# Kernel optimization log

Measured on AMD Instinct MI355X. Metric: run time of the kernel, lower is better.

The kernel has to match this reference:

```python
import jax, jax.numpy as jnp
import numpy as np

N = 100000
E = 800000
IN_CH = 128
HID = 32
HEADS = 8
OUT_CH = 40
NEG_SLOPE = 0.2


def setup_inputs() -> dict:
    key = jax.random.key(0)
    ks = jax.random.split(key, 10)
    x = jax.random.normal(ks[0], (N, IN_CH), dtype=jnp.float32)
    edge_index = jax.random.randint(ks[1], (2, E), 0, N, dtype=jnp.int64)
    # GATConv layer 1: in -> heads*hid, concat=True
    s1 = 1.0 / np.sqrt(IN_CH)
    W1 = jax.random.uniform(ks[2], (IN_CH, HEADS * HID), jnp.float32, -s1, s1)
    att_src1 = jax.random.uniform(ks[3], (1, HEADS, HID), jnp.float32, -s1, s1)
    att_dst1 = jax.random.uniform(ks[4], (1, HEADS, HID), jnp.float32, -s1, s1)
    b1 = jnp.zeros((HEADS * HID,), jnp.float32)
    # GATConv layer 2: heads*hid -> out, heads=1, concat=True
    s2 = 1.0 / np.sqrt(HEADS * HID)
    W2 = jax.random.uniform(ks[5], (HEADS * HID, OUT_CH), jnp.float32, -s2, s2)
    att_src2 = jax.random.uniform(ks[6], (1, 1, OUT_CH), jnp.float32, -s2, s2)
    att_dst2 = jax.random.uniform(ks[7], (1, 1, OUT_CH), jnp.float32, -s2, s2)
    b2 = jnp.zeros((OUT_CH,), jnp.float32)
    return {"x": x, "edge_index": edge_index,
            "W1": W1, "att_src1": att_src1, "att_dst1": att_dst1, "b1": b1,
            "W2": W2, "att_src2": att_src2, "att_dst2": att_dst2, "b2": b2}


def _gat_layer(x, src, dst, W, att_src, att_dst, bias, heads, out_ch):
    n = x.shape[0]
    xp = (x @ W).reshape(n, heads, out_ch)               # [N,H,C]
    a_src = jnp.sum(xp * att_src, axis=-1)               # [N,H]
    a_dst = jnp.sum(xp * att_dst, axis=-1)               # [N,H]
    logits = a_src[src] + a_dst[dst]                      # [Etot,H]
    logits = jnp.where(logits > 0, logits, NEG_SLOPE * logits)  # leaky_relu
    # segment softmax over destination node
    m = jax.ops.segment_max(logits, dst, num_segments=n)  # [N,H]
    p = jnp.exp(logits - m[dst])
    z = jax.ops.segment_sum(p, dst, num_segments=n)
    alpha = p / (z[dst] + 1e-16)                           # [Etot,H]
    out = jax.ops.segment_sum(xp[src] * alpha[:, :, None], dst, num_segments=n)
    return out.reshape(n, heads * out_ch) + bias


def reference(x, edge_index, W1, att_src1, att_dst1, b1, W2, att_src2, att_dst2, b2):
    n = x.shape[0]
    # add self loops (PyG GATConv default add_self_loops=True)
    loop = jnp.arange(n, dtype=edge_index.dtype)
    src = jnp.concatenate([edge_index[0], loop])
    dst = jnp.concatenate([edge_index[1], loop])
    # dropout p=0.2 is identity in eval mode
    h = _gat_layer(x, src, dst, W1, att_src1, att_dst1, b1, HEADS, HID)
    h = jax.nn.relu(h)
    out = _gat_layer(h, src, dst, W2, att_src2, att_dst2, b2, 1, OUT_CH)
    return jax.nn.log_softmax(out, axis=1)
```

## Files before the change

kernel.cpp:

```cpp
#include <hip/hip_runtime.h>
#include <math.h>

#define NN 100000
#define NE 800000
#define C1 256
#define OC 40
#define XPAD 64
#define NEG 0.2f
#define FCHUNK 4096
#define G1BLK 782

typedef _Float16 h4 __attribute__((ext_vector_type(4)));
typedef _Float16 h8 __attribute__((ext_vector_type(8)));
typedef float f4v __attribute__((ext_vector_type(4)));
typedef float f2v __attribute__((ext_vector_type(2)));

static __device__ __forceinline__ float leaky(float v){ return v > 0.f ? v : NEG*v; }

static __device__ __forceinline__ h8 mk8(float4 a, float4 b){
  h8 r = {(_Float16)a.x,(_Float16)a.y,(_Float16)a.z,(_Float16)a.w,
          (_Float16)b.x,(_Float16)b.y,(_Float16)b.z,(_Float16)b.w};
  return r;
}

static __device__ __forceinline__ void gload_lds16h(const _Float16* g, _Float16* l){
  __builtin_amdgcn_global_load_lds((const __attribute__((address_space(1))) void*)g,
                                   (__attribute__((address_space(3))) void*)l, 16, 0, 0);
}


__global__ __launch_bounds__(256) void k_wt(const float* __restrict__ W1, const float* __restrict__ W2,
                                            const float* __restrict__ aS1, const float* __restrict__ aD1,
                                            const float* __restrict__ aS2, const float* __restrict__ aD2,
                                            _Float16* __restrict__ W1s, _Float16* __restrict__ W2t,
                                            int* __restrict__ deg){
  int b = blockIdx.x;
  if (b < 128){
    int k = b, c = threadIdx.x;
    W1s[(size_t)c*128 + (((k>>3) ^ (c&15))<<3) + (k&7)] = (_Float16)W1[k*256 + c];
  } else if (b < 176){
    int nb = b - 128;
    int e = threadIdx.x;
    int l = e >> 2, j = e & 3;
    int k = (l>>5)*128 + ((l>>4)&1)*64 + j*16 + (l&15);
    float v = (nb < OC) ? W2[(size_t)k*OC + nb] : 0.f;
    W2t[(size_t)nb*256 + e] = (_Float16)v;
  } else if (b < 178){
    int b2 = b - 176;
    int h  = threadIdx.x >> 5;
    int kb = (threadIdx.x & 31) * 4;
    const float* att = b2 ? aD1 : aS1;
    const int c = 256 + b2*8 + h;
    #pragma unroll
    for (int kk = 0; kk < 4; ++kk){
      int k = kb + kk;
      float s = 0.f;
      for (int cc = 0; cc < 32; ++cc) s += W1[k*256 + h*32 + cc] * att[h*32 + cc];
      W1s[(size_t)c*128 + (((k>>3) ^ (c&15))<<3) + (k&7)] = (_Float16)s;
    }
  } else if (b < 194){
    int j = b - 178;
    int e = threadIdx.x;
    int l = e >> 2, jj = e & 3;
    int k = (l>>5)*128 + ((l>>4)&1)*64 + jj*16 + (l&15);
    float v = 0.f;
    if (j == 0){ for (int c = 0; c < OC; ++c) v += W2[(size_t)k*OC + c] * aS2[c]; }
    else if (j == 1){ for (int c = 0; c < OC; ++c) v += W2[(size_t)k*OC + c] * aD2[c]; }
    W2t[(size_t)(48 + j)*256 + e] = (_Float16)v;
  } else {
    int i = (b - 194)*256 + threadIdx.x;
    if (i < NN) deg[i] = 1;
  }
}

__global__ __launch_bounds__(512, 4) void k_gemm1(const float* __restrict__ x,
    const _Float16* __restrict__ W1s, unsigned* __restrict__ xp1w,
    float* __restrict__ asrc, float* __restrict__ adst,
    const int* __restrict__ ei, int* __restrict__ deg)
{
  __shared__ _Float16 bs[272*128];
  if (blockIdx.x >= G1BLK){
    int i = (blockIdx.x - G1BLK)*512 + threadIdx.x;
    if (i < NE) atomicAdd(&deg[ei[NE + i]], 1);
    return;
  }
  const int tid  = threadIdx.x;
  const int lane = tid & 63;
  const int w    = tid >> 6;
  const int n = lane & 15, quad = lane >> 4;
  const int r0 = blockIdx.x * 128 + w*16;

  #pragma unroll
  for (int it = 0; it < 8; ++it){
    int idx = it*512 + tid;
    gload_lds16h(W1s + (size_t)idx*8, bs + (size_t)(it*512 + w*64)*8);
  }
  if (w < 4){
    int idx = 4096 + w*64 + lane;
    gload_lds16h(W1s + (size_t)idx*8, bs + (size_t)(4096 + w*64)*8);
  }

  int ra = r0 + n; ra = ra < NN ? ra : NN-1;
  const float* xr = x + (size_t)ra*128 + quad*8;
  float4 fa[4][2];
  #pragma unroll
  for (int ks = 0; ks < 4; ++ks){
    fa[ks][0] = *(const float4*)(xr + ks*32);
    fa[ks][1] = *(const float4*)(xr + ks*32 + 4);
  }

  __syncthreads();

  f4v acc[17];
  #pragma unroll
  for (int ct = 0; ct < 17; ++ct) acc[ct] = (f4v){0.f,0.f,0.f,0.f};

  #pragma unroll
  for (int ks = 0; ks < 4; ++ks){
    h8 a = mk8(fa[ks][0], fa[ks][1]);
    #pragma unroll
    for (int ct = 0; ct < 17; ++ct){
      const int col = ct*16 + n;
      h8 b = *((const h8*)bs + (size_t)col*16 + (((ks*4 + quad) ^ n)));
      acc[ct] = __builtin_amdgcn_mfma_f32_16x16x32_f16(a, b, acc[ct], 0, 0, 0);
    }
  }

  #pragma unroll
  for (int reg = 0; reg < 4; ++reg){
    const int row = r0 + quad*4 + reg;
    if (row < NN){
      float v[16];
      #pragma unroll
      for (int ct = 0; ct < 16; ++ct) v[ct] = acc[ct][reg];
      unsigned dw0 = (unsigned)__builtin_amdgcn_cvt_pk_fp8_f32(v[0], v[1], 0, false);
      dw0 = (unsigned)__builtin_amdgcn_cvt_pk_fp8_f32(v[2], v[3], (int)dw0, true);
      unsigned dw1 = (unsigned)__builtin_amdgcn_cvt_pk_fp8_f32(v[4], v[5], 0, false);
      dw1 = (unsigned)__builtin_amdgcn_cvt_pk_fp8_f32(v[6], v[7], (int)dw1, true);
      unsigned dw2 = (unsigned)__builtin_amdgcn_cvt_pk_fp8_f32(v[8], v[9], 0, false);
      dw2 = (unsigned)__builtin_amdgcn_cvt_pk_fp8_f32(v[10], v[11], (int)dw2, true);
      unsigned dw3 = (unsigned)__builtin_amdgcn_cvt_pk_fp8_f32(v[12], v[13], 0, false);
      dw3 = (unsigned)__builtin_amdgcn_cvt_pk_fp8_f32(v[14], v[15], (int)dw3, true);
      unsigned* xw = xp1w + (size_t)row*64;
      xw[n]      = dw0;
      xw[16 + n] = dw1;
      xw[32 + n] = dw2;
      xw[48 + n] = dw3;
      float vE = acc[16][reg];
      if (n < 8) asrc[row*8 + n] = vE;
      else       adst[row*8 + (n - 8)] = vE;
    }
  }
}

__global__ __launch_bounds__(256) void k_scan1(const int* __restrict__ deg, int* part, int* bsum){
  __shared__ int lds[256];
  const int t = threadIdx.x;
  const int base = blockIdx.x*1024;
  int v[4]; int s = 0;
  #pragma unroll
  for (int i = 0; i < 4; ++i){ int idx = base + t*4 + i; v[i] = (idx < NN) ? deg[idx] : 0; s += v[i]; }
  lds[t] = s; __syncthreads();
  for (int off = 1; off < 256; off <<= 1){
    int xx = (t >= off) ? lds[t-off] : 0;
    __syncthreads();
    lds[t] += xx;
    __syncthreads();
  }
  int excl = lds[t] - s;
  #pragma unroll
  for (int i = 0; i < 4; ++i){ int idx = base + t*4 + i; if (idx < NN) part[idx] = excl; excl += v[i]; }
  if (t == 255) bsum[blockIdx.x] = lds[255];
}
__global__ void k_scan2(const int* __restrict__ bsum, int* boff){
  const int l = threadIdx.x;
  int a = (l      < 98) ? bsum[l]      : 0;
  int b = (64 + l < 98) ? bsum[64 + l] : 0;
  int sa = a, sb = b;
  #pragma unroll
  for (int off = 1; off < 64; off <<= 1){
    int ta = __shfl_up(sa, off, 64);
    int tb = __shfl_up(sb, off, 64);
    if (l >= off){ sa += ta; sb += tb; }
  }
  const int totalA = __shfl(sa, 63, 64);
  if (l      < 98) boff[l]      = sa - a;
  if (64 + l < 98) boff[64 + l] = totalA + sb - b;
}
__global__ __launch_bounds__(256) void k_scan3(const int* __restrict__ part, const int* __restrict__ boff,
                                               int* rowptr, int* cursor){
  int i = blockIdx.x*256 + threadIdx.x;
  if (i < NN){ int v = part[i] + boff[i >> 10]; rowptr[i] = v; cursor[i] = v; }
  if (i == 0) rowptr[NN] = NN + NE;
}
__global__ __launch_bounds__(256) void k_fill(const int* __restrict__ ei, int* cursor, int* __restrict__ esrc){
  const int xcd = blockIdx.x & 7;
  const int base = (blockIdx.x >> 3) * FCHUNK;
  const int lo = xcd * (NN/8), hi = lo + (NN/8);
  const int end = (base + FCHUNK < NE + NN) ? (base + FCHUNK) : (NE + NN);
  for (int i = base + threadIdx.x; i < end; i += 256){
    int s, d;
    if (i < NE){ s = ei[i]; d = ei[NE + i]; } else { s = d = i - NE; }
    if (d >= lo && d < hi){
      int slot = atomicAdd(&cursor[d], 1);
      esrc[slot] = s;
    }
  }
}

template<int B>
static __device__ __forceinline__ void agg1_batch(
    const int j0, const int je, const int lane,
    const int* __restrict__ esrc, const float* __restrict__ asrc,
    const float adA, const float adB,
    const unsigned* __restrict__ xp1w,
    f2v& accLo, f2v& accHi, float& z0, float& z1)
{
  const int cnt = je - j0;
  const int slot = lane & 15;
  const int hA = (lane >> 4) << 1;
  int idx = j0 + slot; idx = idx < je ? idx : je - 1;
  const int sv = esrc[idx];
  float pv0 = 0.f, pv1 = 0.f;
  if (slot < cnt){
    f2v av = *(const f2v*)(asrc + (size_t)sv*8 + hA);
    pv0 = __expf(leaky(av.x + adA));
    pv1 = __expf(leaky(av.y + adB));
  }
  z0 += pv0; z1 += pv1;
  unsigned u[B];
  #pragma unroll
  for (int e = 0; e < B; ++e){
    int s = __builtin_amdgcn_readlane(sv, e);
    u[e] = xp1w[(size_t)s*64 + lane];
  }
  __builtin_amdgcn_sched_barrier(0);
  const int pb = lane & 48;
  #pragma unroll
  for (int e = 0; e < B; ++e){
    const float pA = __shfl(pv0, pb | e, 64);
    const float pB = __shfl(pv1, pb | e, 64);
    f2v lo = __builtin_amdgcn_cvt_pk_f32_fp8((int)u[e], false);
    f2v hi = __builtin_amdgcn_cvt_pk_f32_fp8((int)u[e], true);
    accLo += (f2v){pA, pA} * lo;
    accHi += (f2v){pB, pB} * hi;
  }
}

__global__ __launch_bounds__(1024) void k_agg1(const unsigned* __restrict__ xp1w,
    const float* __restrict__ asrc, const float* __restrict__ adst,
    const float* __restrict__ b1, const int* __restrict__ rowptr,
    const int* __restrict__ esrc, const _Float16* __restrict__ W2t,
    _Float16* __restrict__ xp2, float* __restrict__ asrc2, float* __restrict__ adst2)
{
  __shared__ _Float16 hs[16*264];
  const int lane = threadIdx.x & 63;
  const int w = threadIdx.x >> 6;
  int n = __builtin_amdgcn_readfirstlane(blockIdx.x*16 + w);
  const int hA = (lane >> 4) << 1;
  const f2v ad = *(const f2v*)(adst + (size_t)n*8 + hA);
  const int jb = rowptr[n], je = rowptr[n+1];
  const int cbase = (lane>>5)*128 + ((lane>>4)&1)*64 + (lane&15);
  const float bp0 = b1[cbase], bp1 = b1[cbase+16], bp2 = b1[cbase+32], bp3 = b1[cbase+48];
  f2v accLo = {0.f,0.f}, accHi = {0.f,0.f};
  float z0 = 0.f, z1 = 0.f;

  int j0 = jb;
  while (j0 < je){
    if (je - j0 > 8){
      agg1_batch<16>(j0, je, lane, esrc, asrc, ad.x, ad.y, xp1w, accLo, accHi, z0, z1);
      j0 += 16;
    } else {
      agg1_batch<8>(j0, je, lane, esrc, asrc, ad.x, ad.y, xp1w, accLo, accHi, z0, z1);
      j0 += 8;
    }
  }
  #pragma unroll
  for (int off = 1; off <= 8; off <<= 1){
    z0 += __shfl_xor(z0, off, 64);
    z1 += __shfl_xor(z1, off, 64);
  }
  const float invA = 1.f/(z0 + 1e-16f), invB = 1.f/(z1 + 1e-16f);
  h4 o = {(_Float16)fmaxf(accLo.x*invA + bp0, 0.f),
          (_Float16)fmaxf(accLo.y*invA + bp1, 0.f),
          (_Float16)fmaxf(accHi.x*invB + bp2, 0.f),
          (_Float16)fmaxf(accHi.y*invB + bp3, 0.f)};
  ((h4*)(hs + (size_t)w*264))[lane] = o;

  __syncthreads();

  if (w < 4){
    const int nq = lane & 15, quad = lane >> 4;
    f4v acc = (f4v){0.f,0.f,0.f,0.f};
    #pragma unroll
    for (int ks = 0; ks < 8; ++ks){
      h8 a = *(const h8*)(hs + (size_t)nq*264 + ks*32 + quad*8);
      h8 b = *(const h8*)(W2t + (size_t)(w*16 + nq)*256 + ks*32 + quad*8);
      acc = __builtin_amdgcn_mfma_f32_16x16x32_f16(a, b, acc, 0, 0, 0);
    }
    const int nb = __builtin_amdgcn_readfirstlane(blockIdx.x*16);
    #pragma unroll
    for (int reg = 0; reg < 4; ++reg){
      const int row = nb + quad*4 + reg;
      float v = acc[reg];
      _Float16* xr = xp2 + (size_t)row*XPAD;
      if (w == 0)      xr[nq]      = (_Float16)v;
      else if (w == 1) xr[16 + nq] = (_Float16)v;
      else if (w == 2){ if (nq < 8) xr[32 + nq] = (_Float16)v; }
      else { if (nq == 0) asrc2[row] = v; else if (nq == 1) adst2[row] = v; }
    }
  }
}

__global__ __launch_bounds__(256) void k_agg2(const _Float16* __restrict__ xp2,
    const float* __restrict__ asrc2, const float* __restrict__ adst2,
    const float* __restrict__ b2, const int* __restrict__ rowptr,
    const int* __restrict__ esrc, float* __restrict__ out)
{
  const int lane = threadIdx.x & 63;
  const int g = lane >> 4;
  const int t = lane & 15;
  int n = __builtin_amdgcn_readfirstlane(blockIdx.x*4 + (threadIdx.x >> 6));
  const float ad = adst2[n];
  const int jb = rowptr[n], je = rowptr[n+1];
  f4v acc = {0.f,0.f,0.f,0.f};
  float zacc = 0.f;

  for (int j0 = jb; j0 < je; j0 += 16){
    const int cnt = je - j0;
    int idx = j0 + t; idx = idx < je ? idx : je - 1;
    const int sv = esrc[idx];
    const float pv = (t < cnt) ? __expf(leaky(asrc2[sv] + ad)) : 0.f;
    zacc += pv;
    h4 u[4];
    #pragma unroll
    for (int e4 = 0; e4 < 4; ++e4){
      int svg = __shfl(sv, e4*4 + g, 64);
      u[e4] = *(const h4*)(xp2 + (size_t)svg*XPAD + t*4);
    }
    __builtin_amdgcn_sched_barrier(0);
    #pragma unroll
    for (int e4 = 0; e4 < 4; ++e4){
      const float p = __shfl(pv, e4*4 + g, 64);
      acc.x += p*(float)u[e4].x;
      acc.y += p*(float)u[e4].y;
      acc.z += p*(float)u[e4].z;
      acc.w += p*(float)u[e4].w;
    }
  }
  #pragma unroll
  for (int off = 1; off <= 8; off <<= 1) zacc += __shfl_xor(zacc, off, 64);
  #pragma unroll
  for (int off = 16; off <= 32; off <<= 1){
    acc.x += __shfl_xor(acc.x, off, 64);
    acc.y += __shfl_xor(acc.y, off, 64);
    acc.z += __shfl_xor(acc.z, off, 64);
    acc.w += __shfl_xor(acc.w, off, 64);
  }
  const float inv = 1.f/(zacc + 1e-16f);
  const bool act = t < 10;
  float4 bv = act ? *(const float4*)(b2 + 4*t) : make_float4(0.f,0.f,0.f,0.f);
  float v0 = acc.x*inv + bv.x, v1 = acc.y*inv + bv.y;
  float v2 = acc.z*inv + bv.z, v3 = acc.w*inv + bv.w;
  float m = act ? fmaxf(fmaxf(v0,v1), fmaxf(v2,v3)) : -INFINITY;
  #pragma unroll
  for (int off = 1; off <= 8; off <<= 1) m = fmaxf(m, __shfl_xor(m, off, 64));
  float es = act ? (__expf(v0-m)+__expf(v1-m)+__expf(v2-m)+__expf(v3-m)) : 0.f;
  #pragma unroll
  for (int off = 1; off <= 8; off <<= 1) es += __shfl_xor(es, off, 64);
  if (lane < 10){
    float lse = m + __logf(es);
    float4 o = make_float4(v0-lse, v1-lse, v2-lse, v3-lse);
    *(float4*)(out + (size_t)n*OC + 4*t) = o;
  }
}

extern "C" void kernel_launch(void* const* d_in, const int* in_sizes, int n_in,
                              void* d_out, int out_size, void* d_ws, size_t ws_size,
                              hipStream_t stream)
{
  const float* x   = (const float*)d_in[0];
  const int*   ei  = (const int*)  d_in[1];
  const float* W1  = (const float*)d_in[2];
  const float* aS1 = (const float*)d_in[3];
  const float* aD1 = (const float*)d_in[4];
  const float* b1  = (const float*)d_in[5];
  const float* W2  = (const float*)d_in[6];
  const float* aS2 = (const float*)d_in[7];
  const float* aD2 = (const float*)d_in[8];
  const float* b2  = (const float*)d_in[9];
  float* out = (float*)d_out;

  char* wsp = (char*)d_ws;
  size_t off = 0;
  auto alloc = [&](size_t bytes){ void* p = wsp + off; off += (bytes + 255) & ~(size_t)255; return p; };
  unsigned* xp1w = (unsigned*)alloc((size_t)NN*C1);
  float* as1  = (float*)alloc((size_t)NN*8*4);
  float* ad1  = (float*)alloc((size_t)NN*8*4);
  float* as2  = (float*)alloc((size_t)NN*4);
  float* ad2  = (float*)alloc((size_t)NN*4);
  int* deg    = (int*)alloc((size_t)NN*4);
  int* part   = (int*)alloc((size_t)NN*4);
  int* rowptr = (int*)alloc((size_t)(NN+1)*4);
  int* cursor = (int*)alloc((size_t)NN*4);
  int* bsum   = (int*)alloc(98*4);
  int* boff   = (int*)alloc(98*4);
  int* esrc   = (int*)alloc((size_t)(NN+NE)*4);
  _Float16* W1s = (_Float16*)alloc((size_t)272*128*2);
  _Float16* W2t = (_Float16*)alloc((size_t)64*256*2);
  _Float16* xp2 = (_Float16*)alloc((size_t)NN*XPAD*2);
  (void)ws_size; (void)in_sizes; (void)n_in; (void)out_size;

  const int fill_chunks = (NE + NN + FCHUNK - 1) / FCHUNK;
  const int deg_blocks  = (NE + 511) / 512;

  k_wt    <<<194 + (NN + 255)/256, 256, 0, stream>>>(W1, W2, aS1, aD1, aS2, aD2, W1s, W2t, deg);
  k_gemm1 <<<G1BLK + deg_blocks,   512, 0, stream>>>(x, W1s, xp1w, as1, ad1, ei, deg);
  k_scan1 <<<98,   256, 0, stream>>>(deg, part, bsum);
  k_scan2 <<<1,    64,  0, stream>>>(bsum, boff);
  k_scan3 <<<391,  256, 0, stream>>>(part, boff, rowptr, cursor);
  k_fill  <<<fill_chunks*8, 256, 0, stream>>>(ei, cursor, esrc);
  k_agg1  <<<6250, 1024, 0, stream>>>(xp1w, as1, ad1, b1, rowptr, esrc, W2t, xp2, as2, ad2);
  k_agg2  <<<25000,256, 0, stream>>>(xp2, as2, ad2, b2, rowptr, esrc, out);
}
```

Measured before the change: 308.5 us.

## Sort nodes by in-degree bucket to balance aggregation warps

Builds a degree histogram during the scan, prefix-sums it, and produces a permutation of nodes grouped by in-degree (capped at 63). Both aggregation kernels then process nodes in that permuted order, so the waves in a block handle similar edge counts and spend less time idling on divergent loop lengths. This adds histogram atomics, a perm array and an extra indirection. Nodes sharing a block are no longer adjacent, so layer-2 output writes become scattered and reads of destination-side data lose locality.

```diff
diff --git a/kernel.cpp b/kernel.cpp
--- a/kernel.cpp
+++ b/kernel.cpp
@@ -33,7 +33,7 @@
                                             const float* __restrict__ aS1, const float* __restrict__ aD1,
                                             const float* __restrict__ aS2, const float* __restrict__ aD2,
                                             _Float16* __restrict__ W1s, _Float16* __restrict__ W2t,
-                                            int* __restrict__ deg){
+                                            int* __restrict__ deg, int* __restrict__ hbin){
   int b = blockIdx.x;
   if (b < 128){
     int k = b, c = threadIdx.x;
@@ -70,6 +70,7 @@
   } else {
     int i = (b - 194)*256 + threadIdx.x;
     if (i < NN) deg[i] = 1;
+    if (b == 194 && threadIdx.x < 64) hbin[threadIdx.x] = 0;
   }
 }
 
@@ -153,14 +154,22 @@
   }
 }
 
-__global__ __launch_bounds__(256) void k_scan1(const int* __restrict__ deg, int* part, int* bsum){
+__global__ __launch_bounds__(256) void k_scan1(const int* __restrict__ deg, int* part, int* bsum,
+                                               int* __restrict__ hbin){
   __shared__ int lds[256];
+  __shared__ int lh[64];
   const int t = threadIdx.x;
+  if (t < 64) lh[t] = 0;
   const int base = blockIdx.x*1024;
   int v[4]; int s = 0;
   #pragma unroll
   for (int i = 0; i < 4; ++i){ int idx = base + t*4 + i; v[i] = (idx < NN) ? deg[idx] : 0; s += v[i]; }
   lds[t] = s; __syncthreads();
+  #pragma unroll
+  for (int i = 0; i < 4; ++i){
+    int idx = base + t*4 + i;
+    if (idx < NN) atomicAdd(&lh[v[i] < 63 ? v[i] : 63], 1);
+  }
   for (int off = 1; off < 256; off <<= 1){
     int xx = (t >= off) ? lds[t-off] : 0;
     __syncthreads();
@@ -171,8 +180,11 @@
   #pragma unroll
   for (int i = 0; i < 4; ++i){ int idx = base + t*4 + i; if (idx < NN) part[idx] = excl; excl += v[i]; }
   if (t == 255) bsum[blockIdx.x] = lds[255];
-}
-__global__ void k_scan2(const int* __restrict__ bsum, int* boff){
+  __syncthreads();
+  if (t < 64 && lh[t] > 0) atomicAdd(&hbin[t], lh[t]);
+}
+__global__ void k_scan2(const int* __restrict__ bsum, int* boff,
+                        const int* __restrict__ hbin, int* __restrict__ hcur){
   const int l = threadIdx.x;
   int a = (l      < 98) ? bsum[l]      : 0;
   int b = (64 + l < 98) ? bsum[64 + l] : 0;
@@ -186,12 +198,37 @@
   const int totalA = __shfl(sa, 63, 64);
   if (l      < 98) boff[l]      = sa - a;
   if (64 + l < 98) boff[64 + l] = totalA + sb - b;
+  int hb = hbin[l];
+  int sh = hb;
+  #pragma unroll
+  for (int off = 1; off < 64; off <<= 1){
+    int th = __shfl_up(sh, off, 64);
+    if (l >= off) sh += th;
+  }
+  hcur[l] = sh - hb;
 }
 __global__ __launch_bounds__(256) void k_scan3(const int* __restrict__ part, const int* __restrict__ boff,
-                                               int* rowptr, int* cursor){
-  int i = blockIdx.x*256 + threadIdx.x;
-  if (i < NN){ int v = part[i] + boff[i >> 10]; rowptr[i] = v; cursor[i] = v; }
+                                               const int* __restrict__ deg,
+                                               int* rowptr, int* cursor,
+                                               int* __restrict__ hcur, int* __restrict__ perm){
+  __shared__ int lrank[64];
+  __shared__ int lbase[64];
+  const int t = threadIdx.x;
+  if (t < 64) lrank[t] = 0;
+  __syncthreads();
+  int i = blockIdx.x*256 + t;
+  const bool ok = i < NN;
+  int bin = 0, rank = 0;
+  if (ok){
+    int v = part[i] + boff[i >> 10]; rowptr[i] = v; cursor[i] = v;
+    int d = deg[i]; bin = d < 63 ? d : 63;
+    rank = atomicAdd(&lrank[bin], 1);
+  }
   if (i == 0) rowptr[NN] = NN + NE;
+  __syncthreads();
+  if (t < 64 && lrank[t] > 0) lbase[t] = atomicAdd(&hcur[t], lrank[t]);
+  __syncthreads();
+  if (ok) perm[lbase[bin] + rank] = i;
 }
 __global__ __launch_bounds__(256) void k_fill(const int* __restrict__ ei, int* cursor, int* __restrict__ esrc){
   const int xcd = blockIdx.x & 7;
@@ -250,13 +287,16 @@
 __global__ __launch_bounds__(1024) void k_agg1(const unsigned* __restrict__ xp1w,
     const float* __restrict__ asrc, const float* __restrict__ adst,
     const float* __restrict__ b1, const int* __restrict__ rowptr,
-    const int* __restrict__ esrc, const _Float16* __restrict__ W2t,
+    const int* __restrict__ esrc, const int* __restrict__ perm,
+    const _Float16* __restrict__ W2t,
     _Float16* __restrict__ xp2, float* __restrict__ asrc2, float* __restrict__ adst2)
 {
   __shared__ _Float16 hs[16*264];
+  __shared__ int pperm[16];
   const int lane = threadIdx.x & 63;
   const int w = threadIdx.x >> 6;
-  int n = __builtin_amdgcn_readfirstlane(blockIdx.x*16 + w);
+  int n = __builtin_amdgcn_readfirstlane(perm[blockIdx.x*16 + w]);
+  if (lane == 0) pperm[w] = n;
   const int hA = (lane >> 4) << 1;
   const f2v ad = *(const f2v*)(adst + (size_t)n*8 + hA);
   const int jb = rowptr[n], je = rowptr[n+1];
@@ -298,10 +338,9 @@
       h8 b = *(const h8*)(W2t + (size_t)(w*16 + nq)*256 + ks*32 + quad*8);
       acc = __builtin_amdgcn_mfma_f32_16x16x32_f16(a, b, acc, 0, 0, 0);
     }
-    const int nb = __builtin_amdgcn_readfirstlane(blockIdx.x*16);
     #pragma unroll
     for (int reg = 0; reg < 4; ++reg){
-      const int row = nb + quad*4 + reg;
+      const int row = pperm[quad*4 + reg];
       float v = acc[reg];
       _Float16* xr = xp2 + (size_t)row*XPAD;
       if (w == 0)      xr[nq]      = (_Float16)v;
@@ -315,12 +354,13 @@
 __global__ __launch_bounds__(256) void k_agg2(const _Float16* __restrict__ xp2,
     const float* __restrict__ asrc2, const float* __restrict__ adst2,
     const float* __restrict__ b2, const int* __restrict__ rowptr,
-    const int* __restrict__ esrc, float* __restrict__ out)
+    const int* __restrict__ esrc, const int* __restrict__ perm,
+    float* __restrict__ out)
 {
   const int lane = threadIdx.x & 63;
   const int g = lane >> 4;
   const int t = lane & 15;
-  int n = __builtin_amdgcn_readfirstlane(blockIdx.x*4 + (threadIdx.x >> 6));
+  int n = __builtin_amdgcn_readfirstlane(perm[blockIdx.x*4 + (threadIdx.x >> 6)]);
   const float ad = adst2[n];
   const int jb = rowptr[n], je = rowptr[n+1];
   f4v acc = {0.f,0.f,0.f,0.f};
@@ -405,6 +445,9 @@
   int* cursor = (int*)alloc((size_t)NN*4);
   int* bsum   = (int*)alloc(98*4);
   int* boff   = (int*)alloc(98*4);
+  int* hbin   = (int*)alloc(64*4);
+  int* hcur   = (int*)alloc(64*4);
+  int* perm   = (int*)alloc((size_t)NN*4);
   int* esrc   = (int*)alloc((size_t)(NN+NE)*4);
   _Float16* W1s = (_Float16*)alloc((size_t)272*128*2);
   _Float16* W2t = (_Float16*)alloc((size_t)64*256*2);
@@ -414,12 +457,12 @@
   const int fill_chunks = (NE + NN + FCHUNK - 1) / FCHUNK;
   const int deg_blocks  = (NE + 511) / 512;
 
-  k_wt    <<<194 + (NN + 255)/256, 256, 0, stream>>>(W1, W2, aS1, aD1, aS2, aD2, W1s, W2t, deg);
+  k_wt    <<<194 + (NN + 255)/256, 256, 0, stream>>>(W1, W2, aS1, aD1, aS2, aD2, W1s, W2t, deg, hbin);
   k_gemm1 <<<G1BLK + deg_blocks,   512, 0, stream>>>(x, W1s, xp1w, as1, ad1, ei, deg);
-  k_scan1 <<<98,   256, 0, stream>>>(deg, part, bsum);
-  k_scan2 <<<1,    64,  0, stream>>>(bsum, boff);
-  k_scan3 <<<391,  256, 0, stream>>>(part, boff, rowptr, cursor);
+  k_scan1 <<<98,   256, 0, stream>>>(deg, part, bsum, hbin);
+  k_scan2 <<<1,    64,  0, stream>>>(bsum, boff, hbin, hcur);
+  k_scan3 <<<391,  256, 0, stream>>>(part, boff, deg, rowptr, cursor, hcur, perm);
   k_fill  <<<fill_chunks*8, 256, 0, stream>>>(ei, cursor, esrc);
-  k_agg1  <<<6250, 1024, 0, stream>>>(xp1w, as1, ad1, b1, rowptr, esrc, W2t, xp2, as2, ad2);
-  k_agg2  <<<25000,256, 0, stream>>>(xp2, as2, ad2, b2, rowptr, esrc, out);
-}
+  k_agg1  <<<6250, 1024, 0, stream>>>(xp1w, as1, ad1, b1, rowptr, esrc, perm, W2t, xp2, as2, ad2);
+  k_agg2  <<<25000,256, 0, stream>>>(xp2, as2, ad2, b2, rowptr, esrc, perm, out);
+}
```

Result: slower. 329.2 us (+6.7%).

## Sort nodes by degree within 256-node tiles to balance agg1 wavefronts

Applied to the files above, without the earlier changes.

k_scan3 now builds a per-256-node-block counting sort of nodes by in-degree (capped at 63) and writes a permutation. k_agg1 reads its node id through this permutation, so the 16 waves of a block handle nodes of similar degree and less time is lost waiting on the longest wave at the block barrier. Output rows for the MFMA projection are scattered through the permutation held in shared memory. The cost is an extra perm array, a shared-memory atomic histogram in scan3, less locality in node order, and scattered xp2 writes.

```diff
diff --git a/kernel.cpp b/kernel.cpp
--- a/kernel.cpp
+++ b/kernel.cpp
@@ -188,10 +188,34 @@
   if (64 + l < 98) boff[64 + l] = totalA + sb - b;
 }
 __global__ __launch_bounds__(256) void k_scan3(const int* __restrict__ part, const int* __restrict__ boff,
-                                               int* rowptr, int* cursor){
-  int i = blockIdx.x*256 + threadIdx.x;
-  if (i < NN){ int v = part[i] + boff[i >> 10]; rowptr[i] = v; cursor[i] = v; }
+                                               const int* __restrict__ deg,
+                                               int* rowptr, int* cursor, int* __restrict__ perm){
+  __shared__ int lh[64];
+  __shared__ int lbase[64];
+  const int t = threadIdx.x;
+  if (t < 64) lh[t] = 0;
+  __syncthreads();
+  int i = blockIdx.x*256 + t;
+  const bool ok = i < NN;
+  int bin = 0, rank = 0;
+  if (ok){
+    int v = part[i] + boff[i >> 10]; rowptr[i] = v; cursor[i] = v;
+    int d = deg[i]; bin = d < 63 ? d : 63;
+    rank = atomicAdd(&lh[bin], 1);
+  }
   if (i == 0) rowptr[NN] = NN + NE;
+  __syncthreads();
+  if (t < 64){
+    int hb = lh[t], sh = hb;
+    #pragma unroll
+    for (int off = 1; off < 64; off <<= 1){
+      int th = __shfl_up(sh, off, 64);
+      if (t >= off) sh += th;
+    }
+    lbase[t] = sh - hb;
+  }
+  __syncthreads();
+  if (ok) perm[blockIdx.x*256 + lbase[bin] + rank] = i;
 }
 __global__ __launch_bounds__(256) void k_fill(const int* __restrict__ ei, int* cursor, int* __restrict__ esrc){
   const int xcd = blockIdx.x & 7;
@@ -250,13 +274,16 @@
 __global__ __launch_bounds__(1024) void k_agg1(const unsigned* __restrict__ xp1w,
     const float* __restrict__ asrc, const float* __restrict__ adst,
     const float* __restrict__ b1, const int* __restrict__ rowptr,
-    const int* __restrict__ esrc, const _Float16* __restrict__ W2t,
+    const int* __restrict__ esrc, const int* __restrict__ perm,
+    const _Float16* __restrict__ W2t,
     _Float16* __restrict__ xp2, float* __restrict__ asrc2, float* __restrict__ adst2)
 {
   __shared__ _Float16 hs[16*264];
+  __shared__ int pperm[16];
   const int lane = threadIdx.x & 63;
   const int w = threadIdx.x >> 6;
-  int n = __builtin_amdgcn_readfirstlane(blockIdx.x*16 + w);
+  int n = __builtin_amdgcn_readfirstlane(perm[blockIdx.x*16 + w]);
+  if (lane == 0) pperm[w] = n;
   const int hA = (lane >> 4) << 1;
   const f2v ad = *(const f2v*)(adst + (size_t)n*8 + hA);
   const int jb = rowptr[n], je = rowptr[n+1];
@@ -298,10 +325,9 @@
       h8 b = *(const h8*)(W2t + (size_t)(w*16 + nq)*256 + ks*32 + quad*8);
       acc = __builtin_amdgcn_mfma_f32_16x16x32_f16(a, b, acc, 0, 0, 0);
     }
-    const int nb = __builtin_amdgcn_readfirstlane(blockIdx.x*16);
     #pragma unroll
     for (int reg = 0; reg < 4; ++reg){
-      const int row = nb + quad*4 + reg;
+      const int row = pperm[quad*4 + reg];
       float v = acc[reg];
       _Float16* xr = xp2 + (size_t)row*XPAD;
       if (w == 0)      xr[nq]      = (_Float16)v;
@@ -405,6 +431,7 @@
   int* cursor = (int*)alloc((size_t)NN*4);
   int* bsum   = (int*)alloc(98*4);
   int* boff   = (int*)alloc(98*4);
+  int* perm   = (int*)alloc((size_t)NN*4);
   int* esrc   = (int*)alloc((size_t)(NN+NE)*4);
   _Float16* W1s = (_Float16*)alloc((size_t)272*128*2);
   _Float16* W2t = (_Float16*)alloc((size_t)64*256*2);
@@ -418,8 +445,8 @@
   k_gemm1 <<<G1BLK + deg_blocks,   512, 0, stream>>>(x, W1s, xp1w, as1, ad1, ei, deg);
   k_scan1 <<<98,   256, 0, stream>>>(deg, part, bsum);
   k_scan2 <<<1,    64,  0, stream>>>(bsum, boff);
-  k_scan3 <<<391,  256, 0, stream>>>(part, boff, rowptr, cursor);
+  k_scan3 <<<391,  256, 0, stream>>>(part, boff, deg, rowptr, cursor, perm);
   k_fill  <<<fill_chunks*8, 256, 0, stream>>>(ei, cursor, esrc);
-  k_agg1  <<<6250, 1024, 0, stream>>>(xp1w, as1, ad1, b1, rowptr, esrc, W2t, xp2, as2, ad2);
+  k_agg1  <<<6250, 1024, 0, stream>>>(xp1w, as1, ad1, b1, rowptr, esrc, perm, W2t, xp2, as2, ad2);
   k_agg2  <<<25000,256, 0, stream>>>(xp2, as2, ad2, b2, rowptr, esrc, out);
 }
```

After: 330.5 us. 7.1% more time.
